# Performance work log

Hardware: AMD Instinct MI355X
Metric: run time of the kernel (lower is better)

## Reference

```python
import jax, jax.numpy as jnp
import numpy as np

NEG_SLOPE = 0.2


def _gat_conv(x, edge_index, W, a_src, a_dst, b, heads, out_ch, concat):
    N = x.shape[0]
    # add self loops (PyG GATConv default)
    loops = jnp.arange(N, dtype=edge_index.dtype)
    src = jnp.concatenate([edge_index[0], loops])
    dst = jnp.concatenate([edge_index[1], loops])

    h = (x @ W).reshape(N, heads, out_ch)            # [N,H,C]
    alpha_s = jnp.einsum('nhc,hc->nh', h, a_src)     # [N,H]
    alpha_d = jnp.einsum('nhc,hc->nh', h, a_dst)     # [N,H]
    e = jax.nn.leaky_relu(alpha_s[src] + alpha_d[dst], NEG_SLOPE)  # [E,H]

    # softmax over incoming edges of each dst node (every node has a self loop)
    m = jax.ops.segment_max(e, dst, num_segments=N)  # [N,H]
    e = jnp.exp(e - m[dst])
    denom = jax.ops.segment_sum(e, dst, num_segments=N)  # [N,H]
    alpha = e / denom[dst]                           # [E,H]

    out = jax.ops.segment_sum(h[src] * alpha[..., None], dst, num_segments=N)  # [N,H,C]
    out = out.reshape(N, heads * out_ch) if concat else out.mean(axis=1)
    return out + b


def setup_inputs() -> dict:
    key = jax.random.key(0)
    ks = jax.random.split(key, 12)
    N, E = 100000, 3200000
    F_IN, HID, H1, H2, NCLS = 7, 8, 8, 1, 2
    x = jax.random.normal(ks[0], (N, F_IN), dtype=jnp.float32)
    edge_index = jax.random.randint(ks[1], (2, E), 0, N, dtype=jnp.int64)
    s1 = 1.0 / np.sqrt(F_IN)
    s2 = 1.0 / np.sqrt(HID * H1)
    return {
        'x': x,
        'edge_index': edge_index,
        'W1': jax.random.uniform(ks[2], (F_IN, H1 * HID), jnp.float32, -s1, s1),
        'a_src1': jax.random.uniform(ks[3], (H1, HID), jnp.float32, -s1, s1),
        'a_dst1': jax.random.uniform(ks[4], (H1, HID), jnp.float32, -s1, s1),
        'b1': jnp.zeros((H1 * HID,), jnp.float32),
        'W2': jax.random.uniform(ks[5], (H1 * HID, H2 * NCLS), jnp.float32, -s2, s2),
        'a_src2': jax.random.uniform(ks[6], (H2, NCLS), jnp.float32, -s2, s2),
        'a_dst2': jax.random.uniform(ks[7], (H2, NCLS), jnp.float32, -s2, s2),
        'b2': jnp.zeros((NCLS,), jnp.float32),
    }


def reference(x, edge_index, W1, a_src1, a_dst1, b1, W2, a_src2, a_dst2, b2):
    # eval mode: dropout is identity
    h = _gat_conv(x, edge_index, W1, a_src1, a_dst1, b1, heads=8, out_ch=8, concat=True)
    h = jax.nn.elu(h)
    out = _gat_conv(h, edge_index, W2, a_src2, a_dst2, b2, heads=1, out_ch=2, concat=False)
    return jax.nn.log_softmax(out, axis=1)
```

## Files before the change

### kernel.cpp

```cpp
#include <hip/hip_runtime.h>
#include <math.h>

#define NEG_SLOPE 0.2f
#define L2E 1.4426950408889634f
#define NPB_SHIFT 8
#define NBMAX 512
#define SC_EDGES 16384
#define SC_THREADS 1024
#define CAP 9216

__device__ __forceinline__ unsigned short f2bf(float f) {
    unsigned int u = __float_as_uint(f);
    u += 0x7FFFu + ((u >> 16) & 1u);
    return (unsigned short)(u >> 16);
}

__global__ void k_h1_scatter(const float* __restrict__ x, const float* __restrict__ W1,
                             const float* __restrict__ a_src, const float* __restrict__ a_dst,
                             int N, char* __restrict__ rec,
                             float* __restrict__ as1, float* __restrict__ ad1,
                             const int* __restrict__ srcA, const int* __restrict__ dstA,
                             int E, int sb, int* __restrict__ cursor_g,
                             unsigned int* __restrict__ payload) {
    __shared__ union {
        struct { int hist[NBMAX]; int gbase[NBMAX]; } sc;
        float ws[7 * 64];
    } smem;
    int t = threadIdx.x;

    if ((int)blockIdx.x < sb) {
        const int ITER = SC_EDGES / SC_THREADS;
        unsigned pay[ITER];
        int meta[ITER];
        int base = blockIdx.x * SC_EDGES;
        int cnt = E - base; if (cnt > SC_EDGES) cnt = SC_EDGES;
        for (int i = t; i < NBMAX; i += SC_THREADS) smem.sc.hist[i] = 0;
        __syncthreads();
#pragma unroll
        for (int k = 0; k < ITER; ++k) {
            int j = k * SC_THREADS + t;
            if (j < cnt) {
                int d = dstA[base + j];
                int s = srcA[base + j];
                int b = d >> NPB_SHIFT;
                pay[k] = ((unsigned int)(d & ((1 << NPB_SHIFT) - 1)) << 24) | (unsigned int)s;
                int r = atomicAdd(&smem.sc.hist[b], 1);
                meta[k] = (b << 15) | r;
            } else {
                meta[k] = -1;
            }
        }
        __syncthreads();
        for (int b = t; b < NBMAX; b += SC_THREADS) {
            int c = smem.sc.hist[b];
            smem.sc.gbase[b] = c ? atomicAdd(&cursor_g[b], c) : 0;
        }
        __syncthreads();
#pragma unroll
        for (int k = 0; k < ITER; ++k) {
            if (meta[k] >= 0) {
                int b = meta[k] >> 15;
                int r = meta[k] & 0x7FFF;
                int pos = smem.sc.gbase[b] + r;
                if ((unsigned)pos < CAP)
                    payload[(size_t)b * CAP + pos] = pay[k];
            }
        }
        return;
    }

    for (int i = t; i < 7 * 64; i += SC_THREADS) smem.ws[i] = W1[i];
    __syncthreads();
    int lane = t & 63;
    int base_n = (blockIdx.x - sb) * 64 + (t >> 6) * 4;
    float asv = a_src[lane];
    float adv = a_dst[lane];
#pragma unroll
    for (int u = 0; u < 4; ++u) {
        int n = base_n + u;
        if (n >= N) break;
        float hv = 0.f;
#pragma unroll
        for (int k = 0; k < 7; ++k) hv += x[n * 7 + k] * smem.ws[k * 64 + lane];
        ((unsigned short*)(rec + ((size_t)n << 7)))[lane] = f2bf(hv);
        float ps = hv * asv;
        float pd = hv * adv;
#pragma unroll
        for (int off = 1; off < 8; off <<= 1) {
            ps += __shfl_xor(ps, off);
            pd += __shfl_xor(pd, off);
        }
        if ((lane & 7) == 0) {
            as1[n * 8 + (lane >> 3)] = ps * L2E;
            ad1[n * 8 + (lane >> 3)] = pd * L2E;
        }
    }
}

__global__ void k_buildcsr(const unsigned int* __restrict__ payload,
                           const int* __restrict__ cursor_g, int N,
                           int* __restrict__ deg, int* __restrict__ rows,
                           int* __restrict__ csr) {
    __shared__ int hist[256], exbase[256], scanb[256];
    const int ITER = (CAP + 1023) / 1024;
    unsigned p[ITER];
    int mt[ITER];
    int b = blockIdx.x;
    int t = threadIdx.x;
    int cntb = cursor_g[b]; if (cntb > CAP) cntb = CAP;
    int bs = b * CAP;
    int nodeBase = b << NPB_SHIFT;
    int nNodes = N - nodeBase; if (nNodes > 256) nNodes = 256;
    if (t < 256) hist[t] = 0;
    __syncthreads();
#pragma unroll
    for (int k = 0; k < ITER; ++k) {
        int i = k * 1024 + t;
        if (i < cntb) {
            p[k] = payload[bs + i];
            int dl = p[k] >> 24;
            int r = atomicAdd(&hist[dl], 1);
            mt[k] = (dl << 14) | r;
        } else {
            mt[k] = -1;
        }
    }
    __syncthreads();
    if (t < 256) scanb[t] = hist[t];
    __syncthreads();
    for (int off = 1; off < 256; off <<= 1) {
        int u = 0;
        if (t < 256 && t >= off) u = scanb[t - off];
        __syncthreads();
        if (t < 256) scanb[t] += u;
        __syncthreads();
    }
    if (t < 256) {
        int own = hist[t];
        int ex = scanb[t] - own;
        exbase[t] = ex;
        if (t < nNodes) { deg[nodeBase + t] = own; rows[nodeBase + t] = bs + ex; }
    }
    __syncthreads();
#pragma unroll
    for (int k = 0; k < ITER; ++k) {
        if (mt[k] >= 0) {
            int dl = mt[k] >> 14;
            int r = mt[k] & 0x3FFF;
            csr[bs + exbase[dl] + r] = (int)(p[k] & 0xFFFFFFu);
        }
    }
}

__device__ __forceinline__ void oct_step(
    const char* __restrict__ rec, const char* __restrict__ as1b,
    int e0, int e1, int e2, int e3, int e4, int e5, int e6, int e7,
    int g, unsigned foff, unsigned aoff, float adv, float wm, bool mask,
    float& den, float& a0, float& a1, float& a2, float& a3,
    float& a4, float& a5, float& a6, float& a7) {
    int sa = (g & 1) ? e1 : e0;
    int sb = (g & 1) ? e3 : e2;
    int sc = (g & 1) ? e5 : e4;
    int sd = (g & 1) ? e7 : e6;
    int sab = (g & 2) ? sb : sa;
    int scd = (g & 2) ? sd : sc;
    int s   = (g & 4) ? scd : sab;
    unsigned u = (unsigned)s;
    uint4 f = *(const uint4*)(rec + (size_t)((u << 7) + foff));
    float al = *(const float*)(as1b + (size_t)((u << 5) + aoff));
    float t = al + adv;
    float w = __builtin_amdgcn_exp2f(fmaxf(t, NEG_SLOPE * t));
    if (mask) w *= wm;
    den += w;
    a0 = fmaf(w, __uint_as_float(f.x << 16), a0);
    a1 = fmaf(w, __uint_as_float(f.x & 0xFFFF0000u), a1);
    a2 = fmaf(w, __uint_as_float(f.y << 16), a2);
    a3 = fmaf(w, __uint_as_float(f.y & 0xFFFF0000u), a3);
    a4 = fmaf(w, __uint_as_float(f.z << 16), a4);
    a5 = fmaf(w, __uint_as_float(f.z & 0xFFFF0000u), a5);
    a6 = fmaf(w, __uint_as_float(f.w << 16), a6);
    a7 = fmaf(w, __uint_as_float(f.w & 0xFFFF0000u), a7);
}

__global__ void k_agg1(const char* __restrict__ rec, const float* __restrict__ as1,
                       const float* __restrict__ ad1,
                       const int* __restrict__ deg, const int* __restrict__ rows,
                       const int* __restrict__ csr, const float* __restrict__ b1,
                       const float* __restrict__ W2, const float* __restrict__ as2w,
                       const float* __restrict__ ad2w, int N,
                       float4* __restrict__ pack) {
    int n = blockIdx.x * 4 + (threadIdx.x >> 6);
    int lane = threadIdx.x & 63;
    if (n >= N) return;
    n = __builtin_amdgcn_readfirstlane(n);
    const char* as1b = (const char*)as1;
    int ql = lane & 7;
    int g  = lane >> 3;
    unsigned foff = (unsigned)(ql << 4);
    unsigned aoff = (unsigned)(ql << 2);
    float adv = ad1[n * 8 + ql];
    int d = __builtin_amdgcn_readfirstlane(deg[n]);
    int start = __builtin_amdgcn_readfirstlane(rows[n]);
    float a0 = 0.f, a1 = 0.f, a2 = 0.f, a3 = 0.f;
    float a4 = 0.f, a5 = 0.f, a6 = 0.f, a7 = 0.f;
    float den = 0.f;
    int c = 0;
    int nfull = d & ~31;
    for (; c < nfull; c += 32) {
        int idxv = csr[start + c + (lane & 31)];
#pragma unroll
        for (int k = 0; k < 4; ++k) {
            int e0 = __builtin_amdgcn_readlane(idxv, 8 * k + 0);
            int e1 = __builtin_amdgcn_readlane(idxv, 8 * k + 1);
            int e2 = __builtin_amdgcn_readlane(idxv, 8 * k + 2);
            int e3 = __builtin_amdgcn_readlane(idxv, 8 * k + 3);
            int e4 = __builtin_amdgcn_readlane(idxv, 8 * k + 4);
            int e5 = __builtin_amdgcn_readlane(idxv, 8 * k + 5);
            int e6 = __builtin_amdgcn_readlane(idxv, 8 * k + 6);
            int e7 = __builtin_amdgcn_readlane(idxv, 8 * k + 7);
            oct_step(rec, as1b, e0, e1, e2, e3, e4, e5, e6, e7, g, foff, aoff,
                     adv, 1.f, false, den, a0, a1, a2, a3, a4, a5, a6, a7);
        }
    }
    for (; c < d; c += 8) {
        int r = d - c; if (r > 8) r = 8;
        int e0 = __builtin_amdgcn_readfirstlane(csr[start + c]);
        int e1 = (r > 1) ? __builtin_amdgcn_readfirstlane(csr[start + c + 1]) : e0;
        int e2 = (r > 2) ? __builtin_amdgcn_readfirstlane(csr[start + c + 2]) : e0;
        int e3 = (r > 3) ? __builtin_amdgcn_readfirstlane(csr[start + c + 3]) : e0;
        int e4 = (r > 4) ? __builtin_amdgcn_readfirstlane(csr[start + c + 4]) : e0;
        int e5 = (r > 5) ? __builtin_amdgcn_readfirstlane(csr[start + c + 5]) : e0;
        int e6 = (r > 6) ? __builtin_amdgcn_readfirstlane(csr[start + c + 6]) : e0;
        int e7 = (r > 7) ? __builtin_amdgcn_readfirstlane(csr[start + c + 7]) : e0;
        float wm = (g < r) ? 1.f : 0.f;
        oct_step(rec, as1b, e0, e1, e2, e3, e4, e5, e6, e7, g, foff, aoff,
                 adv, wm, true, den, a0, a1, a2, a3, a4, a5, a6, a7);
    }
    {
        float wm = (g == 0) ? 1.f : 0.f;
        oct_step(rec, as1b, n, n, n, n, n, n, n, n, g, foff, aoff,
                 adv, wm, true, den, a0, a1, a2, a3, a4, a5, a6, a7);
    }
    den += __shfl_xor(den, 8); den += __shfl_xor(den, 16); den += __shfl_xor(den, 32);
    a0 += __shfl_xor(a0, 8); a0 += __shfl_xor(a0, 16); a0 += __shfl_xor(a0, 32);
    a1 += __shfl_xor(a1, 8); a1 += __shfl_xor(a1, 16); a1 += __shfl_xor(a1, 32);
    a2 += __shfl_xor(a2, 8); a2 += __shfl_xor(a2, 16); a2 += __shfl_xor(a2, 32);
    a3 += __shfl_xor(a3, 8); a3 += __shfl_xor(a3, 16); a3 += __shfl_xor(a3, 32);
    a4 += __shfl_xor(a4, 8); a4 += __shfl_xor(a4, 16); a4 += __shfl_xor(a4, 32);
    a5 += __shfl_xor(a5, 8); a5 += __shfl_xor(a5, 16); a5 += __shfl_xor(a5, 32);
    a6 += __shfl_xor(a6, 8); a6 += __shfl_xor(a6, 16); a6 += __shfl_xor(a6, 32);
    a7 += __shfl_xor(a7, 8); a7 += __shfl_xor(a7, 16); a7 += __shfl_xor(a7, 32);
    float rden = 1.f / den;
    float4 bbA = ((const float4*)b1)[2 * ql];
    float4 bbB = ((const float4*)b1)[2 * ql + 1];
    float o0 = a0 * rden + bbA.x;
    float o1 = a1 * rden + bbA.y;
    float o2 = a2 * rden + bbA.z;
    float o3 = a3 * rden + bbA.w;
    float o4 = a4 * rden + bbB.x;
    float o5 = a5 * rden + bbB.y;
    float o6 = a6 * rden + bbB.z;
    float o7 = a7 * rden + bbB.w;
    float v0 = o0 > 0.f ? o0 : (__expf(o0) - 1.f);
    float v1 = o1 > 0.f ? o1 : (__expf(o1) - 1.f);
    float v2 = o2 > 0.f ? o2 : (__expf(o2) - 1.f);
    float v3 = o3 > 0.f ? o3 : (__expf(o3) - 1.f);
    float v4 = o4 > 0.f ? o4 : (__expf(o4) - 1.f);
    float v5 = o5 > 0.f ? o5 : (__expf(o5) - 1.f);
    float v6 = o6 > 0.f ? o6 : (__expf(o6) - 1.f);
    float v7 = o7 > 0.f ? o7 : (__expf(o7) - 1.f);
    const float4* W2v = (const float4*)W2;
    float4 w20 = W2v[4 * ql + 0];
    float4 w21 = W2v[4 * ql + 1];
    float4 w22 = W2v[4 * ql + 2];
    float4 w23 = W2v[4 * ql + 3];
    float p0 = v0 * w20.x + v1 * w20.z + v2 * w21.x + v3 * w21.z
             + v4 * w22.x + v5 * w22.z + v6 * w23.x + v7 * w23.z;
    float p1 = v0 * w20.y + v1 * w20.w + v2 * w21.y + v3 * w21.w
             + v4 * w22.y + v5 * w22.w + v6 * w23.y + v7 * w23.w;
#pragma unroll
    for (int off = 1; off < 8; off <<= 1) {
        p0 += __shfl_xor(p0, off);
        p1 += __shfl_xor(p1, off);
    }
    if (lane == 0) {
        float4 pk;
        pk.x = p0;
        pk.y = p1;
        pk.z = (p0 * as2w[0] + p1 * as2w[1]) * L2E;
        pk.w = (p0 * ad2w[0] + p1 * ad2w[1]) * L2E;
        pack[n] = pk;
    }
}

__global__ void k_agg2(const float4* __restrict__ pack, const int* __restrict__ deg,
                       const int* __restrict__ rows, const int* __restrict__ csr,
                       const float* __restrict__ b2, int N, float* __restrict__ out) {
    int n = blockIdx.x * 8 + (threadIdx.x >> 5);
    int hl = threadIdx.x & 31;
    if (n >= N) return;
    float4 self = pack[n];
    float adv = self.w;
    int d = deg[n];
    int start = rows[n];
    float den = 0.f, a0 = 0.f, a1 = 0.f;
    for (int i = hl; i < d; i += 32) {
        int src = csr[start + i];
        float4 q = pack[src];
        float t = q.z + adv;
        float w = __builtin_amdgcn_exp2f(fmaxf(t, NEG_SLOPE * t));
        den += w;
        a0 += w * q.x;
        a1 += w * q.y;
    }
#pragma unroll
    for (int off = 1; off < 32; off <<= 1) {
        den += __shfl_xor(den, off);
        a0  += __shfl_xor(a0, off);
        a1  += __shfl_xor(a1, off);
    }
    if (hl == 0) {
        float t = self.z + adv;
        float w = __builtin_amdgcn_exp2f(fmaxf(t, NEG_SLOPE * t));
        den += w;
        a0 += w * self.x;
        a1 += w * self.y;
        float o0 = a0 / den + b2[0];
        float o1 = a1 / den + b2[1];
        float m = fmaxf(o0, o1);
        float lse = m + logf(__expf(o0 - m) + __expf(o1 - m));
        out[n * 2 + 0] = o0 - lse;
        out[n * 2 + 1] = o1 - lse;
    }
}

extern "C" void kernel_launch(void* const* d_in, const int* in_sizes, int n_in,
                              void* d_out, int out_size, void* d_ws, size_t ws_size,
                              hipStream_t stream) {
    const float* x     = (const float*)d_in[0];
    const int*   ei    = (const int*)d_in[1];
    const float* W1    = (const float*)d_in[2];
    const float* as1w  = (const float*)d_in[3];
    const float* ad1w  = (const float*)d_in[4];
    const float* b1    = (const float*)d_in[5];
    const float* W2    = (const float*)d_in[6];
    const float* as2w  = (const float*)d_in[7];
    const float* ad2w  = (const float*)d_in[8];
    const float* b2    = (const float*)d_in[9];
    float* out = (float*)d_out;

    const int N = in_sizes[0] / 7;
    const int E = in_sizes[1] / 2;
    const int* srcA = ei;
    const int* dstA = ei + E;
    const int NB = (N + ((1 << NPB_SHIFT) - 1)) >> NPB_SHIFT;

    size_t off = 0;
    auto alloc = [&](size_t bytes) -> void* {
        void* p = (char*)d_ws + off;
        off += (bytes + 255) & ~(size_t)255;
        return p;
    };
    unsigned int* payload = (unsigned int*)alloc((size_t)NB * CAP * 4);
    char*  rec  = (char*)alloc((size_t)N * 128);
    float* as1  = (float*)alloc((size_t)N * 8 * 4);
    float* ad1  = (float*)alloc((size_t)N * 8 * 4);
    float4* pack = (float4*)alloc((size_t)N * 16);
    int*   deg  = (int*)alloc((size_t)N * 4);
    int*   rows = (int*)alloc((size_t)N * 4);
    int*   csr  = (int*)alloc((size_t)NB * CAP * 4);
    int*   cursor_g = (int*)alloc(NBMAX * 4);

    const int nb2 = (N + 63) / 64;
    const int sb  = (E + SC_EDGES - 1) / SC_EDGES;
    const int nb  = (N + 3) / 4;

    hipMemsetAsync(cursor_g, 0, NBMAX * 4, stream);
    k_h1_scatter<<<sb + nb2, SC_THREADS, 0, stream>>>(x, W1, as1w, ad1w, N, rec, as1, ad1,
                                                      srcA, dstA, E, sb, cursor_g, payload);
    k_buildcsr<<<NB, 1024, 0, stream>>>(payload, cursor_g, N, deg, rows, csr);
    k_agg1<<<nb, 256, 0, stream>>>(rec, as1, ad1, deg, rows, csr, b1,
                                   W2, as2w, ad2w, N, pack);
    k_agg2<<<(N + 7) / 8, 256, 0, stream>>>(pack, deg, rows, csr, b2, N, out);
}
```

Before: 241.0 us.

## Recompute source attention logits from gathered features; pack deg/rows; nontemporal loads

Drops the precomputed per-node source attention logits and instead recomputes them in the aggregation step as a dot product of the gathered bf16 feature row with the a_src weights. This removes one random gather per edge. It also merges the degree and row-start arrays into a single int2 array and marks streaming loads of edges, payload and CSR as nontemporal. The cost is extra FMAs per edge, and the logits now come from bf16-rounded features, which slightly changes numerics.

```diff
diff --git a/kernel.cpp b/kernel.cpp
--- a/kernel.cpp
+++ b/kernel.cpp
@@ -16,9 +16,9 @@
 }
 
 __global__ void k_h1_scatter(const float* __restrict__ x, const float* __restrict__ W1,
-                             const float* __restrict__ a_src, const float* __restrict__ a_dst,
+                             const float* __restrict__ a_dst,
                              int N, char* __restrict__ rec,
-                             float* __restrict__ as1, float* __restrict__ ad1,
+                             float* __restrict__ ad1,
                              const int* __restrict__ srcA, const int* __restrict__ dstA,
                              int E, int sb, int* __restrict__ cursor_g,
                              unsigned int* __restrict__ payload) {
@@ -40,8 +40,8 @@
         for (int k = 0; k < ITER; ++k) {
             int j = k * SC_THREADS + t;
             if (j < cnt) {
-                int d = dstA[base + j];
-                int s = srcA[base + j];
+                int d = __builtin_nontemporal_load(dstA + base + j);
+                int s = __builtin_nontemporal_load(srcA + base + j);
                 int b = d >> NPB_SHIFT;
                 pay[k] = ((unsigned int)(d & ((1 << NPB_SHIFT) - 1)) << 24) | (unsigned int)s;
                 int r = atomicAdd(&smem.sc.hist[b], 1);
@@ -73,7 +73,6 @@
     __syncthreads();
     int lane = t & 63;
     int base_n = (blockIdx.x - sb) * 64 + (t >> 6) * 4;
-    float asv = a_src[lane];
     float adv = a_dst[lane];
 #pragma unroll
     for (int u = 0; u < 4; ++u) {
@@ -83,24 +82,16 @@
 #pragma unroll
         for (int k = 0; k < 7; ++k) hv += x[n * 7 + k] * smem.ws[k * 64 + lane];
         ((unsigned short*)(rec + ((size_t)n << 7)))[lane] = f2bf(hv);
-        float ps = hv * asv;
         float pd = hv * adv;
 #pragma unroll
-        for (int off = 1; off < 8; off <<= 1) {
-            ps += __shfl_xor(ps, off);
-            pd += __shfl_xor(pd, off);
-        }
-        if ((lane & 7) == 0) {
-            as1[n * 8 + (lane >> 3)] = ps * L2E;
-            ad1[n * 8 + (lane >> 3)] = pd * L2E;
-        }
+        for (int off = 1; off < 8; off <<= 1) pd += __shfl_xor(pd, off);
+        if ((lane & 7) == 0) ad1[n * 8 + (lane >> 3)] = pd * L2E;
     }
 }
 
 __global__ void k_buildcsr(const unsigned int* __restrict__ payload,
                            const int* __restrict__ cursor_g, int N,
-                           int* __restrict__ deg, int* __restrict__ rows,
-                           int* __restrict__ csr) {
+                           int2* __restrict__ nrow, int* __restrict__ csr) {
     __shared__ int hist[256], exbase[256], scanb[256];
     const int ITER = (CAP + 1023) / 1024;
     unsigned p[ITER];
@@ -117,7 +108,7 @@
     for (int k = 0; k < ITER; ++k) {
         int i = k * 1024 + t;
         if (i < cntb) {
-            p[k] = payload[bs + i];
+            p[k] = __builtin_nontemporal_load(payload + bs + i);
             int dl = p[k] >> 24;
             int r = atomicAdd(&hist[dl], 1);
             mt[k] = (dl << 14) | r;
@@ -139,7 +130,7 @@
         int own = hist[t];
         int ex = scanb[t] - own;
         exbase[t] = ex;
-        if (t < nNodes) { deg[nodeBase + t] = own; rows[nodeBase + t] = bs + ex; }
+        if (t < nNodes) nrow[nodeBase + t] = make_int2(own, bs + ex);
     }
     __syncthreads();
 #pragma unroll
@@ -153,9 +144,10 @@
 }
 
 __device__ __forceinline__ void oct_step(
-    const char* __restrict__ rec, const char* __restrict__ as1b,
+    const char* __restrict__ rec,
     int e0, int e1, int e2, int e3, int e4, int e5, int e6, int e7,
-    int g, unsigned foff, unsigned aoff, float adv, float wm, bool mask,
+    int g, unsigned foff, float4 awA, float4 awB,
+    float adv, float wm, bool mask,
     float& den, float& a0, float& a1, float& a2, float& a3,
     float& a4, float& a5, float& a6, float& a7) {
     int sa = (g & 1) ? e1 : e0;
@@ -167,24 +159,33 @@
     int s   = (g & 4) ? scd : sab;
     unsigned u = (unsigned)s;
     uint4 f = *(const uint4*)(rec + (size_t)((u << 7) + foff));
-    float al = *(const float*)(as1b + (size_t)((u << 5) + aoff));
+    float f0 = __uint_as_float(f.x << 16);
+    float f1 = __uint_as_float(f.x & 0xFFFF0000u);
+    float f2 = __uint_as_float(f.y << 16);
+    float f3 = __uint_as_float(f.y & 0xFFFF0000u);
+    float f4 = __uint_as_float(f.z << 16);
+    float f5 = __uint_as_float(f.z & 0xFFFF0000u);
+    float f6 = __uint_as_float(f.w << 16);
+    float f7 = __uint_as_float(f.w & 0xFFFF0000u);
+    float al = f0 * awA.x + f1 * awA.y + f2 * awA.z + f3 * awA.w
+             + f4 * awB.x + f5 * awB.y + f6 * awB.z + f7 * awB.w;
     float t = al + adv;
     float w = __builtin_amdgcn_exp2f(fmaxf(t, NEG_SLOPE * t));
     if (mask) w *= wm;
     den += w;
-    a0 = fmaf(w, __uint_as_float(f.x << 16), a0);
-    a1 = fmaf(w, __uint_as_float(f.x & 0xFFFF0000u), a1);
-    a2 = fmaf(w, __uint_as_float(f.y << 16), a2);
-    a3 = fmaf(w, __uint_as_float(f.y & 0xFFFF0000u), a3);
-    a4 = fmaf(w, __uint_as_float(f.z << 16), a4);
-    a5 = fmaf(w, __uint_as_float(f.z & 0xFFFF0000u), a5);
-    a6 = fmaf(w, __uint_as_float(f.w << 16), a6);
-    a7 = fmaf(w, __uint_as_float(f.w & 0xFFFF0000u), a7);
-}
-
-__global__ void k_agg1(const char* __restrict__ rec, const float* __restrict__ as1,
+    a0 = fmaf(w, f0, a0);
+    a1 = fmaf(w, f1, a1);
+    a2 = fmaf(w, f2, a2);
+    a3 = fmaf(w, f3, a3);
+    a4 = fmaf(w, f4, a4);
+    a5 = fmaf(w, f5, a5);
+    a6 = fmaf(w, f6, a6);
+    a7 = fmaf(w, f7, a7);
+}
+
+__global__ void k_agg1(const char* __restrict__ rec, const float* __restrict__ asW,
                        const float* __restrict__ ad1,
-                       const int* __restrict__ deg, const int* __restrict__ rows,
+                       const int2* __restrict__ nrow,
                        const int* __restrict__ csr, const float* __restrict__ b1,
                        const float* __restrict__ W2, const float* __restrict__ as2w,
                        const float* __restrict__ ad2w, int N,
@@ -193,21 +194,24 @@
     int lane = threadIdx.x & 63;
     if (n >= N) return;
     n = __builtin_amdgcn_readfirstlane(n);
-    const char* as1b = (const char*)as1;
     int ql = lane & 7;
     int g  = lane >> 3;
     unsigned foff = (unsigned)(ql << 4);
-    unsigned aoff = (unsigned)(ql << 2);
+    float4 awA = ((const float4*)asW)[2 * ql];
+    float4 awB = ((const float4*)asW)[2 * ql + 1];
+    awA.x *= L2E; awA.y *= L2E; awA.z *= L2E; awA.w *= L2E;
+    awB.x *= L2E; awB.y *= L2E; awB.z *= L2E; awB.w *= L2E;
     float adv = ad1[n * 8 + ql];
-    int d = __builtin_amdgcn_readfirstlane(deg[n]);
-    int start = __builtin_amdgcn_readfirstlane(rows[n]);
+    int2 dr = nrow[n];
+    int d = __builtin_amdgcn_readfirstlane(dr.x);
+    int start = __builtin_amdgcn_readfirstlane(dr.y);
     float a0 = 0.f, a1 = 0.f, a2 = 0.f, a3 = 0.f;
     float a4 = 0.f, a5 = 0.f, a6 = 0.f, a7 = 0.f;
     float den = 0.f;
     int c = 0;
     int nfull = d & ~31;
     for (; c < nfull; c += 32) {
-        int idxv = csr[start + c + (lane & 31)];
+        int idxv = __builtin_nontemporal_load(csr + start + c + (lane & 31));
 #pragma unroll
         for (int k = 0; k < 4; ++k) {
             int e0 = __builtin_amdgcn_readlane(idxv, 8 * k + 0);
@@ -218,27 +222,27 @@
             int e5 = __builtin_amdgcn_readlane(idxv, 8 * k + 5);
             int e6 = __builtin_amdgcn_readlane(idxv, 8 * k + 6);
             int e7 = __builtin_amdgcn_readlane(idxv, 8 * k + 7);
-            oct_step(rec, as1b, e0, e1, e2, e3, e4, e5, e6, e7, g, foff, aoff,
+            oct_step(rec, e0, e1, e2, e3, e4, e5, e6, e7, g, foff, awA, awB,
                      adv, 1.f, false, den, a0, a1, a2, a3, a4, a5, a6, a7);
         }
     }
     for (; c < d; c += 8) {
         int r = d - c; if (r > 8) r = 8;
-        int e0 = __builtin_amdgcn_readfirstlane(csr[start + c]);
-        int e1 = (r > 1) ? __builtin_amdgcn_readfirstlane(csr[start + c + 1]) : e0;
-        int e2 = (r > 2) ? __builtin_amdgcn_readfirstlane(csr[start + c + 2]) : e0;
-        int e3 = (r > 3) ? __builtin_amdgcn_readfirstlane(csr[start + c + 3]) : e0;
-        int e4 = (r > 4) ? __builtin_amdgcn_readfirstlane(csr[start + c + 4]) : e0;
-        int e5 = (r > 5) ? __builtin_amdgcn_readfirstlane(csr[start + c + 5]) : e0;
-        int e6 = (r > 6) ? __builtin_amdgcn_readfirstlane(csr[start + c + 6]) : e0;
-        int e7 = (r > 7) ? __builtin_amdgcn_readfirstlane(csr[start + c + 7]) : e0;
+        int e0 = __builtin_amdgcn_readfirstlane(__builtin_nontemporal_load(csr + start + c));
+        int e1 = (r > 1) ? __builtin_amdgcn_readfirstlane(__builtin_nontemporal_load(csr + start + c + 1)) : e0;
+        int e2 = (r > 2) ? __builtin_amdgcn_readfirstlane(__builtin_nontemporal_load(csr + start + c + 2)) : e0;
+        int e3 = (r > 3) ? __builtin_amdgcn_readfirstlane(__builtin_nontemporal_load(csr + start + c + 3)) : e0;
+        int e4 = (r > 4) ? __builtin_amdgcn_readfirstlane(__builtin_nontemporal_load(csr + start + c + 4)) : e0;
+        int e5 = (r > 5) ? __builtin_amdgcn_readfirstlane(__builtin_nontemporal_load(csr + start + c + 5)) : e0;
+        int e6 = (r > 6) ? __builtin_amdgcn_readfirstlane(__builtin_nontemporal_load(csr + start + c + 6)) : e0;
+        int e7 = (r > 7) ? __builtin_amdgcn_readfirstlane(__builtin_nontemporal_load(csr + start + c + 7)) : e0;
         float wm = (g < r) ? 1.f : 0.f;
-        oct_step(rec, as1b, e0, e1, e2, e3, e4, e5, e6, e7, g, foff, aoff,
+        oct_step(rec, e0, e1, e2, e3, e4, e5, e6, e7, g, foff, awA, awB,
                  adv, wm, true, den, a0, a1, a2, a3, a4, a5, a6, a7);
     }
     {
         float wm = (g == 0) ? 1.f : 0.f;
-        oct_step(rec, as1b, n, n, n, n, n, n, n, n, g, foff, aoff,
+        oct_step(rec, n, n, n, n, n, n, n, n, g, foff, awA, awB,
                  adv, wm, true, den, a0, a1, a2, a3, a4, a5, a6, a7);
     }
     den += __shfl_xor(den, 8); den += __shfl_xor(den, 16); den += __shfl_xor(den, 32);
@@ -293,19 +297,20 @@
     }
 }
 
-__global__ void k_agg2(const float4* __restrict__ pack, const int* __restrict__ deg,
-                       const int* __restrict__ rows, const int* __restrict__ csr,
+__global__ void k_agg2(const float4* __restrict__ pack, const int2* __restrict__ nrow,
+                       const int* __restrict__ csr,
                        const float* __restrict__ b2, int N, float* __restrict__ out) {
     int n = blockIdx.x * 8 + (threadIdx.x >> 5);
     int hl = threadIdx.x & 31;
     if (n >= N) return;
     float4 self = pack[n];
     float adv = self.w;
-    int d = deg[n];
-    int start = rows[n];
+    int2 dr = nrow[n];
+    int d = dr.x;
+    int start = dr.y;
     float den = 0.f, a0 = 0.f, a1 = 0.f;
     for (int i = hl; i < d; i += 32) {
-        int src = csr[start + i];
+        int src = __builtin_nontemporal_load(csr + start + i);
         float4 q = pack[src];
         float t = q.z + adv;
         float w = __builtin_amdgcn_exp2f(fmaxf(t, NEG_SLOPE * t));
@@ -363,11 +368,9 @@
     };
     unsigned int* payload = (unsigned int*)alloc((size_t)NB * CAP * 4);
     char*  rec  = (char*)alloc((size_t)N * 128);
-    float* as1  = (float*)alloc((size_t)N * 8 * 4);
     float* ad1  = (float*)alloc((size_t)N * 8 * 4);
     float4* pack = (float4*)alloc((size_t)N * 16);
-    int*   deg  = (int*)alloc((size_t)N * 4);
-    int*   rows = (int*)alloc((size_t)N * 4);
+    int2*  nrow = (int2*)alloc((size_t)N * 8);
     int*   csr  = (int*)alloc((size_t)NB * CAP * 4);
     int*   cursor_g = (int*)alloc(NBMAX * 4);
 
@@ -376,10 +379,10 @@
     const int nb  = (N + 3) / 4;
 
     hipMemsetAsync(cursor_g, 0, NBMAX * 4, stream);
-    k_h1_scatter<<<sb + nb2, SC_THREADS, 0, stream>>>(x, W1, as1w, ad1w, N, rec, as1, ad1,
+    k_h1_scatter<<<sb + nb2, SC_THREADS, 0, stream>>>(x, W1, ad1w, N, rec, ad1,
                                                       srcA, dstA, E, sb, cursor_g, payload);
-    k_buildcsr<<<NB, 1024, 0, stream>>>(payload, cursor_g, N, deg, rows, csr);
-    k_agg1<<<nb, 256, 0, stream>>>(rec, as1, ad1, deg, rows, csr, b1,
+    k_buildcsr<<<NB, 1024, 0, stream>>>(payload, cursor_g, N, nrow, csr);
+    k_agg1<<<nb, 256, 0, stream>>>(rec, as1w, ad1, nrow, csr, b1,
                                    W2, as2w, ad2w, N, pack);
-    k_agg2<<<(N + 7) / 8, 256, 0, stream>>>(pack, deg, rows, csr, b2, N, out);
-}
+    k_agg2<<<(N + 7) / 8, 256, 0, stream>>>(pack, nrow, csr, b2, N, out);
+}
```

After: 237.6 us. About the same (-1.4%).
